# Kernel optimization log

Hardware: AMD Instinct MI355X
Metric: run time of the kernel (lower is better)

The kernel has to match this reference:

```python
import jax, jax.numpy as jnp
import numpy as np

# Clos factorization for in=out=4096, middle_switch_multiplier=4:
BIN, B1, B2, B3, BOUT = 64, 64, 256, 64, 64
B, C, D = 2, 4096, 4096


def setup_inputs() -> dict:
    key = jax.random.key(0)
    ks = jax.random.split(key, 7)
    k = 1.0 / np.sqrt(D)
    x = jax.random.normal(ks[0], (B, C, D), dtype=jnp.float32)
    # kaiming_uniform(a=sqrt(5)) on [bin,b1,b2]-like tensors ~ uniform(-bound, bound)
    w1 = jax.random.uniform(ks[1], (BIN, B1, B2), jnp.float32, -k, k)
    w2 = jax.random.uniform(ks[2], (B1, B2, B3), jnp.float32, -k, k)
    w3 = jax.random.uniform(ks[3], (B2, B3, BOUT), jnp.float32, -k, k)
    bias1 = jax.random.uniform(ks[4], (B1,), jnp.float32, -k, k)
    bias2 = jax.random.uniform(ks[5], (B2,), jnp.float32, -k, k)
    bias3 = jax.random.uniform(ks[6], (B3,), jnp.float32, -k, k)
    return {"x": x, "w1": w1, "w2": w2, "w3": w3,
            "bias1": bias1, "bias2": bias2, "bias3": bias3}


def reference(x, w1, w2, w3, bias1, bias2, bias3):
    b, c, _ = x.shape
    h = x.reshape(b, c, BIN, B1)                      # [b,c,n=bin,r=b1]
    h = jnp.einsum('bcnr,nrm->bcmr', h, w1) + bias1   # [b,c,b2,b1] + bias over b1
    h = jnp.einsum('bcmr,rmn->bcnm', h, w2) + bias2   # [b,c,b3,b2] + bias over b2
    h = jnp.einsum('bcnm,mro->bcor', h, w3) + bias3   # [b,c,bout,b3] + bias over b3
    return h.reshape(b, c, -1)                        # [b,c,out_features]
```

## Files before the change

kernel.cpp:

```cpp
#include <hip/hip_runtime.h>
#include <stdint.h>
#include <stddef.h>

typedef __bf16 bf16_t;
typedef __bf16 bf16x8 __attribute__((ext_vector_type(8)));
typedef __bf16 bf16x4 __attribute__((ext_vector_type(4)));
typedef float f32x4 __attribute__((ext_vector_type(4)));

#define VMW(n) asm volatile("s_waitcnt vmcnt(" #n ")" ::: "memory")
#define LGKM0 asm volatile("s_waitcnt lgkmcnt(0)" ::: "memory")
#define CFENCE asm volatile("" ::: "memory")
#define RAWBAR              \
  do {                      \
    __builtin_amdgcn_s_barrier(); \
    CFENCE;                 \
  } while (0)

__device__ __forceinline__ void gload_lds16(const void* g, void* l) {
  __builtin_amdgcn_global_load_lds(
      (const __attribute__((address_space(1))) uint32_t*)g,
      (__attribute__((address_space(3))) uint32_t*)l, 16, 0, 0);
}

__global__ __launch_bounds__(256) void w2s_k(const float* __restrict__ w2,
                                             float* __restrict__ w2s) {
  const int r = blockIdx.x, m = threadIdx.x;
  const float4* p = (const float4*)(w2 + ((size_t)(r * 256 + m)) * 64);
  float s = 0.f;
#pragma unroll
  for (int i = 0; i < 16; ++i) {
    float4 v = p[i];
    s += (v.x + v.y) + (v.z + v.w);
  }
  w2s[r * 256 + m] = s;
}

__global__ __launch_bounds__(256) void prep_k(
    const float* __restrict__ w1, const float* __restrict__ w3,
    const float* __restrict__ w2s, const float* __restrict__ bias1,
    const float* __restrict__ bias2, bf16_t* __restrict__ w1t,
    bf16_t* __restrict__ w3pt, float* __restrict__ c2) {
  __shared__ float lds[64][65];
  const int b = blockIdx.x;
  const int t = threadIdx.x;
  if (b == 512) {
    float s = 64.f * bias2[t];
#pragma unroll 8
    for (int r = 0; r < 64; ++r) s += bias1[r] * w2s[r * 256 + t];
    c2[t] = s;
    return;
  }
  if (b < 256) {
    const int k0 = (b >> 2) * 64;
    const int mt = (b & 3) * 64;
#pragma unroll
    for (int it = 0; it < 16; ++it) {
      int idx = t + it * 256;
      int kl = idx >> 6, ml = idx & 63;
      int k = k0 + kl;
      lds[kl][ml] = w1[(size_t)k * 256 + mt + ml] * w2s[(k & 63) * 256 + mt + ml];
    }
    __syncthreads();
#pragma unroll
    for (int it = 0; it < 16; ++it) {
      int idx = t + it * 256;
      int ml = idx >> 6, kl = idx & 63;
      w1t[(size_t)(mt + ml) * 4096 + k0 + kl] = (bf16_t)lds[kl][ml];
    }
    return;
  }
  const int b2 = b - 256;
  const int r = b2 & 63;
  const int mt = (b2 >> 6) * 64;
#pragma unroll
  for (int it = 0; it < 16; ++it) {
    int idx = t + it * 256;
    int ml = idx >> 6, o = idx & 63;
    lds[ml][o] = w3[(size_t)(mt + ml) * 4096 + r * 64 + o];
  }
  __syncthreads();
#pragma unroll
  for (int it = 0; it < 16; ++it) {
    int idx = t + it * 256;
    int o = idx >> 6, ml = idx & 63;
    w3pt[(size_t)(o * 64 + r) * 256 + mt + ml] = (bf16_t)lds[ml][o];
  }
}

__global__ __launch_bounds__(512, 2) void gemm1_k(
    const float* __restrict__ X, const bf16_t* __restrict__ W1T,
    const float* __restrict__ c2, bf16_t* __restrict__ S) {
  __shared__ __align__(16) bf16_t lA[2][32 * 64];
  __shared__ __align__(16) bf16_t lB[2][256 * 64];
  const int tid = threadIdx.x;
  const int lane = tid & 63;
  const int wv = tid >> 6;
  const int bid = (int)blockIdx.x;
  const int mtile = (bid & 7) * 32 + (bid >> 3);
  const size_t m0 = (size_t)mtile * 32;
  const int ar = tid >> 4;
  const int ac = tid & 15;

  f32x4 acc[2][2];
#pragma unroll
  for (int i = 0; i < 2; ++i)
#pragma unroll
    for (int j = 0; j < 2; ++j) acc[i][j] = (f32x4){0.f, 0.f, 0.f, 0.f};

  float4 aX, aY;

  auto issueA = [&](float4& dst, int kt) {
    dst = *(const float4*)(X + (m0 + ar) * 4096 + (size_t)(kt * 64 + ac * 4));
  };
  auto writeA = [&](const float4& src, int buf) {
    int off = ar * 128 + ((ac * 8) ^ ((ar & 7) << 4));
    bf16x4 v;
    v[0] = (bf16_t)src.x;
    v[1] = (bf16_t)src.y;
    v[2] = (bf16_t)src.z;
    v[3] = (bf16_t)src.w;
    *(bf16x4*)((char*)(&lA[buf][0]) + off) = v;
  };
  auto issueB = [&](int buf, int kt) {
#pragma unroll
    for (int i = 0; i < 4; ++i) {
      int row = wv * 32 + i * 8 + (lane >> 3);
      int srckb = ((lane & 7) * 16) ^ ((row & 7) << 4);
      const char* src = (const char*)W1T + (size_t)row * 8192 + (size_t)(kt * 64) * 2 + srckb;
      char* dst = (char*)(&lB[buf][0]) + (wv * 32 + i * 8) * 128;
      gload_lds16(src, dst);
    }
  };
  auto compute = [&](int buf) {
#pragma unroll
    for (int kk = 0; kk < 2; ++kk) {
      const int kb = kk * 64 + ((lane >> 4) * 16);
      bf16x8 af[2], bfr[2];
#pragma unroll
      for (int mf = 0; mf < 2; ++mf) {
        int row = mf * 16 + (lane & 15);
        int off = row * 128 + (kb ^ ((row & 7) << 4));
        af[mf] = *(const bf16x8*)((const char*)(&lA[buf][0]) + off);
      }
#pragma unroll
      for (int nf = 0; nf < 2; ++nf) {
        int row = wv * 32 + nf * 16 + (lane & 15);
        int off = row * 128 + (kb ^ ((row & 7) << 4));
        bfr[nf] = *(const bf16x8*)((const char*)(&lB[buf][0]) + off);
      }
#pragma unroll
      for (int mf = 0; mf < 2; ++mf)
#pragma unroll
        for (int nf = 0; nf < 2; ++nf)
          acc[mf][nf] = __builtin_amdgcn_mfma_f32_16x16x32_bf16(af[mf], bfr[nf], acc[mf][nf], 0, 0, 0);
    }
  };

  issueB(0, 0);
  CFENCE;
  issueA(aX, 0);
  CFENCE;
  issueB(1, 1);
  CFENCE;
  issueA(aY, 1);
  CFENCE;
  VMW(5);
  writeA(aX, 0);
  LGKM0;
  RAWBAR;

#pragma unroll 1
  for (int t2 = 0; t2 < 62; t2 += 2) {
    compute(0);
    RAWBAR;
    issueB(0, t2 + 2);
    CFENCE;
    issueA(aX, t2 + 2);
    CFENCE;
    VMW(5);
    writeA(aY, 1);
    LGKM0;
    RAWBAR;
    compute(1);
    RAWBAR;
    issueB(1, t2 + 3);
    CFENCE;
    issueA(aY, t2 + 3);
    CFENCE;
    VMW(5);
    writeA(aX, 0);
    LGKM0;
    RAWBAR;
  }
  compute(0);
  RAWBAR;
  VMW(0);
  writeA(aY, 1);
  LGKM0;
  RAWBAR;
  compute(1);

#pragma unroll
  for (int nf = 0; nf < 2; ++nf) {
    int col = wv * 32 + nf * 16 + (lane & 15);
    float cadd = c2[col];
#pragma unroll
    for (int mf = 0; mf < 2; ++mf) {
#pragma unroll
      for (int q = 0; q < 4; ++q) {
        int row = mf * 16 + (lane >> 4) * 4 + q;
        S[(m0 + row) * 256 + (size_t)col] = (bf16_t)(acc[mf][nf][q] + cadd);
      }
    }
  }
}

__global__ __launch_bounds__(512, 2) void gemm2_k(
    const bf16_t* __restrict__ S, const bf16_t* __restrict__ W3pT,
    const float* __restrict__ bias3, float* __restrict__ OUT) {
  __shared__ __align__(16) bf16_t lA[2][128 * 64];
  __shared__ __align__(16) bf16_t lB[2][256 * 64];
  const int tid = threadIdx.x;
  const int lane = tid & 63;
  const int wv = tid >> 6;
  const int bid = (int)blockIdx.x;
  const int xcd = bid & 7;
  const int rest = bid >> 3;
  const int mt = xcd * 8 + (rest >> 4);
  const int nt = rest & 15;
  const size_t m0 = (size_t)mt * 128;
  const int n0 = nt * 256;
  const int wm = wv >> 2, wn = wv & 3;

  f32x4 acc[4][4];
#pragma unroll
  for (int i = 0; i < 4; ++i)
#pragma unroll
    for (int j = 0; j < 4; ++j) acc[i][j] = (f32x4){0.f, 0.f, 0.f, 0.f};

  auto stage = [&](int buf, int kt) {
#pragma unroll
    for (int i = 0; i < 2; ++i) {
      int row = wv * 16 + i * 8 + (lane >> 3);
      int srckb = ((lane & 7) * 16) ^ ((row & 7) << 4);
      const char* srcA = (const char*)S + (m0 + row) * 512 + (size_t)(kt * 128) + srckb;
      char* dstA = (char*)(&lA[buf][0]) + (wv * 16 + i * 8) * 128;
      gload_lds16(srcA, dstA);
    }
#pragma unroll
    for (int i = 0; i < 4; ++i) {
      int row = wv * 32 + i * 8 + (lane >> 3);
      int srckb = ((lane & 7) * 16) ^ ((row & 7) << 4);
      const char* srcB = (const char*)W3pT + (size_t)(n0 + row) * 512 + (size_t)(kt * 128) + srckb;
      char* dstB = (char*)(&lB[buf][0]) + (wv * 32 + i * 8) * 128;
      gload_lds16(srcB, dstB);
    }
  };
  auto compute = [&](int buf) {
#pragma unroll
    for (int kk = 0; kk < 2; ++kk) {
      const int kb = kk * 64 + ((lane >> 4) * 16);
      bf16x8 af[4], bfr[4];
#pragma unroll
      for (int mf = 0; mf < 4; ++mf) {
        int row = wm * 64 + mf * 16 + (lane & 15);
        int off = row * 128 + (kb ^ ((row & 7) << 4));
        af[mf] = *(const bf16x8*)((const char*)(&lA[buf][0]) + off);
      }
#pragma unroll
      for (int nf = 0; nf < 4; ++nf) {
        int row = wn * 64 + nf * 16 + (lane & 15);
        int off = row * 128 + (kb ^ ((row & 7) << 4));
        bfr[nf] = *(const bf16x8*)((const char*)(&lB[buf][0]) + off);
      }
#pragma unroll
      for (int mf = 0; mf < 4; ++mf)
#pragma unroll
        for (int nf = 0; nf < 4; ++nf)
          acc[mf][nf] = __builtin_amdgcn_mfma_f32_16x16x32_bf16(af[mf], bfr[nf], acc[mf][nf], 0, 0, 0);
    }
  };

  stage(0, 0);
  CFENCE;
  stage(1, 1);
  CFENCE;
  VMW(6);
  RAWBAR;
  compute(0);
  RAWBAR;
  stage(0, 2);
  CFENCE;
  VMW(6);
  RAWBAR;
  compute(1);
  RAWBAR;
  stage(1, 3);
  CFENCE;
  VMW(6);
  RAWBAR;
  compute(0);
  RAWBAR;
  VMW(0);
  RAWBAR;
  compute(1);

#pragma unroll
  for (int nf = 0; nf < 4; ++nf) {
    int jcol = wn * 64 + nf * 16 + (lane & 15);
    float b3 = bias3[jcol & 63];
    int j = n0 + jcol;
#pragma unroll
    for (int mf = 0; mf < 4; ++mf) {
#pragma unroll
      for (int q = 0; q < 4; ++q) {
        size_t row = m0 + (size_t)(wm * 64 + mf * 16 + (lane >> 4) * 4 + q);
        OUT[row * 4096 + j] = acc[mf][nf][q] + b3;
      }
    }
  }
}

extern "C" void kernel_launch(void* const* d_in, const int* in_sizes, int n_in,
                              void* d_out, int out_size, void* d_ws, size_t ws_size,
                              hipStream_t stream) {
  (void)in_sizes; (void)n_in; (void)out_size; (void)ws_size;
  const float* x  = (const float*)d_in[0];
  const float* w1 = (const float*)d_in[1];
  const float* w2 = (const float*)d_in[2];
  const float* w3 = (const float*)d_in[3];
  const float* b1 = (const float*)d_in[4];
  const float* b2 = (const float*)d_in[5];
  const float* b3 = (const float*)d_in[6];
  float* out = (float*)d_out;
  char* ws = (char*)d_ws;

  float*  w2s  = (float*)(ws + 0);
  float*  c2   = (float*)(ws + 65536);
  bf16_t* w1t  = (bf16_t*)(ws + 69632);
  bf16_t* w3pt = (bf16_t*)(ws + 69632 + 2097152);
  bf16_t* S    = (bf16_t*)(ws + 69632 + 2 * 2097152);

  w2s_k<<<64, 256, 0, stream>>>(w2, w2s);
  prep_k<<<513, 256, 0, stream>>>(w1, w3, w2s, b1, b2, w1t, w3pt, c2);
  gemm1_k<<<256, 512, 0, stream>>>(x, w1t, c2, S);
  gemm2_k<<<1024, 512, 0, stream>>>(S, w3pt, b3, out);
}
```

Measured before the change: 128.6 us.

## Retile gemm1 to 64x64 blocks with 256 threads and simpler double buffering

gemm1 moves from 512-thread blocks covering 32 rows by all 256 columns to 256-thread blocks covering 64 rows by 64 columns, launching 512 blocks instead of 256. The hand-scheduled two-stage loop with explicit vmcnt/lgkmcnt waits becomes a plain double-buffered loop: it prefetches tile kt+1, computes tile kt, writes A to LDS, then syncs. The goal is more blocks per CU and a better A/B tile ratio. The cost is that each block reads the fp32 X rows once per column tile, so X is read four times instead of once, and the fine-grained overlap control is lost.

```diff
diff --git a/kernel.cpp b/kernel.cpp
--- a/kernel.cpp
+++ b/kernel.cpp
@@ -8,7 +8,6 @@
 typedef float f32x4 __attribute__((ext_vector_type(4)));
 
 #define VMW(n) asm volatile("s_waitcnt vmcnt(" #n ")" ::: "memory")
-#define LGKM0 asm volatile("s_waitcnt lgkmcnt(0)" ::: "memory")
 #define CFENCE asm volatile("" ::: "memory")
 #define RAWBAR              \
   do {                      \
@@ -87,19 +86,23 @@
   }
 }
 
-__global__ __launch_bounds__(512, 2) void gemm1_k(
+__global__ __launch_bounds__(256, 4) void gemm1_k(
     const float* __restrict__ X, const bf16_t* __restrict__ W1T,
     const float* __restrict__ c2, bf16_t* __restrict__ S) {
-  __shared__ __align__(16) bf16_t lA[2][32 * 64];
-  __shared__ __align__(16) bf16_t lB[2][256 * 64];
+  __shared__ __align__(16) bf16_t lA[2][64 * 64];
+  __shared__ __align__(16) bf16_t lB[2][64 * 64];
   const int tid = threadIdx.x;
   const int lane = tid & 63;
   const int wv = tid >> 6;
   const int bid = (int)blockIdx.x;
-  const int mtile = (bid & 7) * 32 + (bid >> 3);
-  const size_t m0 = (size_t)mtile * 32;
-  const int ar = tid >> 4;
-  const int ac = tid & 15;
+  const int xcd = bid & 7;
+  const int rest = bid >> 3;
+  const int mtile = xcd * 16 + (rest >> 2);
+  const int n0 = (rest & 3) * 64;
+  const size_t m0 = (size_t)mtile * 64;
+  const int wm = wv >> 1, wn = wv & 1;
+  const int ar = tid >> 2;
+  const int acg = tid & 3;
 
   f32x4 acc[2][2];
 #pragma unroll
@@ -107,27 +110,35 @@
 #pragma unroll
     for (int j = 0; j < 2; ++j) acc[i][j] = (f32x4){0.f, 0.f, 0.f, 0.f};
 
-  float4 aX, aY;
-
-  auto issueA = [&](float4& dst, int kt) {
-    dst = *(const float4*)(X + (m0 + ar) * 4096 + (size_t)(kt * 64 + ac * 4));
-  };
-  auto writeA = [&](const float4& src, int buf) {
-    int off = ar * 128 + ((ac * 8) ^ ((ar & 7) << 4));
-    bf16x4 v;
-    v[0] = (bf16_t)src.x;
-    v[1] = (bf16_t)src.y;
-    v[2] = (bf16_t)src.z;
-    v[3] = (bf16_t)src.w;
-    *(bf16x4*)((char*)(&lA[buf][0]) + off) = v;
+  float4 aR[4];
+
+  auto issueA = [&](int kt) {
+#pragma unroll
+    for (int j = 0; j < 4; ++j) {
+      int f4 = acg + j * 4;
+      aR[j] = *(const float4*)(X + (m0 + ar) * 4096 + (size_t)(kt * 64 + f4 * 4));
+    }
+  };
+  auto writeA = [&](int buf) {
+#pragma unroll
+    for (int j = 0; j < 4; ++j) {
+      int f4 = acg + j * 4;
+      int off = ar * 128 + ((f4 * 8) ^ ((ar & 7) << 4));
+      bf16x4 v;
+      v[0] = (bf16_t)aR[j].x;
+      v[1] = (bf16_t)aR[j].y;
+      v[2] = (bf16_t)aR[j].z;
+      v[3] = (bf16_t)aR[j].w;
+      *(bf16x4*)((char*)(&lA[buf][0]) + off) = v;
+    }
   };
   auto issueB = [&](int buf, int kt) {
 #pragma unroll
-    for (int i = 0; i < 4; ++i) {
-      int row = wv * 32 + i * 8 + (lane >> 3);
+    for (int i = 0; i < 2; ++i) {
+      int row = wv * 16 + i * 8 + (lane >> 3);
       int srckb = ((lane & 7) * 16) ^ ((row & 7) << 4);
-      const char* src = (const char*)W1T + (size_t)row * 8192 + (size_t)(kt * 64) * 2 + srckb;
-      char* dst = (char*)(&lB[buf][0]) + (wv * 32 + i * 8) * 128;
+      const char* src = (const char*)W1T + (size_t)(n0 + row) * 8192 + (size_t)(kt * 128) + srckb;
+      char* dst = (char*)(&lB[buf][0]) + (wv * 16 + i * 8) * 128;
       gload_lds16(src, dst);
     }
   };
@@ -138,13 +149,13 @@
       bf16x8 af[2], bfr[2];
 #pragma unroll
       for (int mf = 0; mf < 2; ++mf) {
-        int row = mf * 16 + (lane & 15);
+        int row = wm * 32 + mf * 16 + (lane & 15);
         int off = row * 128 + (kb ^ ((row & 7) << 4));
         af[mf] = *(const bf16x8*)((const char*)(&lA[buf][0]) + off);
       }
 #pragma unroll
       for (int nf = 0; nf < 2; ++nf) {
-        int row = wv * 32 + nf * 16 + (lane & 15);
+        int row = wn * 32 + nf * 16 + (lane & 15);
         int off = row * 128 + (kb ^ ((row & 7) << 4));
         bfr[nf] = *(const bf16x8*)((const char*)(&lB[buf][0]) + off);
       }
@@ -156,59 +167,33 @@
     }
   };
 
+  issueA(0);
   issueB(0, 0);
-  CFENCE;
-  issueA(aX, 0);
-  CFENCE;
-  issueB(1, 1);
-  CFENCE;
-  issueA(aY, 1);
-  CFENCE;
-  VMW(5);
-  writeA(aX, 0);
-  LGKM0;
-  RAWBAR;
+  writeA(0);
+  __syncthreads();
 
 #pragma unroll 1
-  for (int t2 = 0; t2 < 62; t2 += 2) {
-    compute(0);
-    RAWBAR;
-    issueB(0, t2 + 2);
-    CFENCE;
-    issueA(aX, t2 + 2);
-    CFENCE;
-    VMW(5);
-    writeA(aY, 1);
-    LGKM0;
-    RAWBAR;
-    compute(1);
-    RAWBAR;
-    issueB(1, t2 + 3);
-    CFENCE;
-    issueA(aY, t2 + 3);
-    CFENCE;
-    VMW(5);
-    writeA(aX, 0);
-    LGKM0;
-    RAWBAR;
-  }
-  compute(0);
-  RAWBAR;
-  VMW(0);
-  writeA(aY, 1);
-  LGKM0;
-  RAWBAR;
-  compute(1);
+  for (int kt = 0; kt < 64; ++kt) {
+    int cur = kt & 1;
+    bool more = (kt + 1) < 64;
+    if (more) {
+      issueA(kt + 1);
+      issueB(cur ^ 1, kt + 1);
+    }
+    compute(cur);
+    if (more) writeA(cur ^ 1);
+    __syncthreads();
+  }
 
 #pragma unroll
   for (int nf = 0; nf < 2; ++nf) {
-    int col = wv * 32 + nf * 16 + (lane & 15);
+    int col = n0 + wn * 32 + nf * 16 + (lane & 15);
     float cadd = c2[col];
 #pragma unroll
     for (int mf = 0; mf < 2; ++mf) {
 #pragma unroll
       for (int q = 0; q < 4; ++q) {
-        int row = mf * 16 + (lane >> 4) * 4 + q;
+        int row = wm * 32 + mf * 16 + (lane >> 4) * 4 + q;
         S[(m0 + row) * 256 + (size_t)col] = (bf16_t)(acc[mf][nf][q] + cadd);
       }
     }
@@ -343,6 +328,6 @@
 
   w2s_k<<<64, 256, 0, stream>>>(w2, w2s);
   prep_k<<<513, 256, 0, stream>>>(w1, w3, w2s, b1, b2, w1t, w3pt, c2);
-  gemm1_k<<<256, 512, 0, stream>>>(x, w1t, c2, S);
+  gemm1_k<<<512, 256, 0, stream>>>(x, w1t, c2, S);
   gemm2_k<<<1024, 512, 0, stream>>>(S, w3pt, b3, out);
 }
```

Result: faster. 123.3 us (-4.1%).
